# Kernel optimization log

Measured on AMD Instinct MI355X. Metric: run time of the kernel, lower is better.

The kernel has to match this reference:

```python
import jax, jax.numpy as jnp
import numpy as np

B, L, E = 16, 2048, 256


def setup_inputs() -> dict:
    key = jax.random.key(0)
    ks = jax.random.split(key, 8)
    s = 1.0 / np.sqrt(E)
    x = jax.random.normal(ks[0], (B, L, E), dtype=jnp.float32)
    lengths = jax.random.randint(ks[1], (B,), 0, L, dtype=jnp.int32)
    Wq = jax.random.normal(ks[2], (E, E), dtype=jnp.float32) * s
    bq = jax.random.normal(ks[3], (E,), dtype=jnp.float32) * s
    Wk = jax.random.normal(ks[4], (E, E), dtype=jnp.float32) * s
    bk = jax.random.normal(ks[5], (E,), dtype=jnp.float32) * s
    Wv = jax.random.normal(ks[6], (E, E), dtype=jnp.float32) * s
    bv = jax.random.normal(ks[7], (E,), dtype=jnp.float32) * s
    return {"x": x, "lengths": lengths, "Wq": Wq, "bq": bq,
            "Wk": Wk, "bk": bk, "Wv": Wv, "bv": bv}


def reference(x, lengths, Wq, bq, Wk, bk, Wv, bv):
    # ragged validity mask: [B, L, 1]
    mask = (jnp.arange(L)[None, :] < lengths[:, None]).astype(x.dtype)[..., None]
    q = (jnp.einsum('ble,fe->blf', x, Wq) + bq) * mask  # masked queries -> zero padded output rows
    k = (jnp.einsum('ble,fe->blf', x, Wk) + bk) * mask  # masked keys -> exclude padding from contraction
    v = jnp.einsum('ble,fe->blf', x, Wv) + bv           # invalid keys already zeroed via k
    attn_weights = jnp.einsum('bqe,bke->bqk', q, k)      # [B, L, L] (no softmax in original)
    attn_output = jnp.einsum('bqk,bke->bqe', attn_weights, v)  # [B, L, E]
    # to_padded_tensor(pad=0).mean(dim=1) divides by the PADDED length L
    return attn_output.sum(axis=1) / jnp.asarray(L, x.dtype)  # [B, E]
```

## Files before the change

kernel.cpp:

```cpp
#include <hip/hip_runtime.h>

#define Bb 16
#define Ll 2048
#define Ee 256
#define E4 64
#define BPB 32
#define RPB 64
#define JT 16
#define FS (Ee / JT)

#define P1_OFF 0
#define TP_OFF (P1_OFF + Bb*BPB*Ee)
#define C_OFF  (TP_OFF + Bb*JT*Ee)
#define U_OFF  (C_OFF + Bb)
#define W_OFF  (U_OFF + Bb*Ee)

__global__ void __launch_bounds__(256) k1(const float* __restrict__ x,
                                          const int* __restrict__ lengths,
                                          float* __restrict__ P1) {
    const int b = blockIdx.y, i = blockIdx.x;
    const int tid = threadIdx.x, lane = tid & 63, wid = tid >> 6;
    const int len = lengths[b];
    const int r0 = i * RPB;
    float4* slot = (float4*)(P1 + ((size_t)(b * BPB + i)) * Ee);
    if (r0 >= len) {
        if (tid < 64) slot[tid] = make_float4(0.f, 0.f, 0.f, 0.f);
        return;
    }
    const float4* xb = (const float4*)(x + (size_t)b * Ll * Ee);
    float4 acc = {0.f, 0.f, 0.f, 0.f};
#pragma unroll
    for (int rr = 0; rr < 16; ++rr) {
        const int r = r0 + wid + rr * 4;
        float4 v = xb[(size_t)r * E4 + lane];
        const bool ok = (r < len);
        acc.x += ok ? v.x : 0.f; acc.y += ok ? v.y : 0.f;
        acc.z += ok ? v.z : 0.f; acc.w += ok ? v.w : 0.f;
    }
    __shared__ float4 part[256];
    part[tid] = acc;
    __syncthreads();
    if (tid < 64) {
        float4 a = part[tid], b1 = part[64+tid], c1 = part[128+tid], d1 = part[192+tid];
        slot[tid] = make_float4(a.x+b1.x+c1.x+d1.x, a.y+b1.y+c1.y+d1.y,
                                a.z+b1.z+c1.z+d1.z, a.w+b1.w+c1.w+d1.w);
    }
}

__global__ void __launch_bounds__(256) k2(const float* __restrict__ P1,
                                          const int* __restrict__ lengths,
                                          const float* __restrict__ Wq,
                                          const float* __restrict__ bq,
                                          const float* __restrict__ Wk,
                                          const float* __restrict__ bk,
                                          float* __restrict__ TP, float* __restrict__ C,
                                          float* __restrict__ U, float* __restrict__ W) {
    const int b = blockIdx.y, j = blockIdx.x;
    const int tid = threadIdx.x;
    const int len = lengths[b];
    __shared__ alignas(16) float xs[Ee];
    __shared__ alignas(16) float s_sh[Ee];
    {
        const float* P = P1 + (size_t)b * BPB * Ee + tid;
        float a0 = 0.f, a1 = 0.f, a2 = 0.f, a3 = 0.f;
#pragma unroll
        for (int q = 0; q < BPB; q += 4) {
            a0 += P[(size_t)(q+0) * Ee];
            a1 += P[(size_t)(q+1) * Ee];
            a2 += P[(size_t)(q+2) * Ee];
            a3 += P[(size_t)(q+3) * Ee];
        }
        xs[tid] = (a0 + a1) + (a2 + a3);
    }
    __syncthreads();
    {
        const float4* wrow = (const float4*)(Wq + (size_t)tid * Ee);
        const float4* x4   = (const float4*)xs;
        float acc = 0.f;
#pragma unroll 8
        for (int q = 0; q < E4; ++q) {
            float4 w = wrow[q]; float4 v = x4[q];
            acc += w.x*v.x + w.y*v.y + w.z*v.z + w.w*v.w;
        }
        s_sh[tid] = acc + (float)len * bq[tid];
    }
    __syncthreads();
    float tp = 0.f;
#pragma unroll
    for (int f0 = 0; f0 < FS; ++f0) {
        const int f = j * FS + f0;
        tp += s_sh[f] * Wk[(size_t)f * Ee + tid];
    }
    TP[((size_t)(b * JT + j)) * Ee + tid] = tp;
    if (j == 0) {
        U[b * Ee + tid] = 0.f;
        float p = s_sh[tid] * bk[tid];
#pragma unroll
        for (int m = 32; m; m >>= 1) p += __shfl_xor(p, m, 64);
        __shared__ float cred[4];
        if ((tid & 63) == 0) cred[tid >> 6] = p;
        __syncthreads();
        if (tid == 0) { C[b] = cred[0] + cred[1] + cred[2] + cred[3]; W[b] = 0.f; }
    }
}

__global__ void __launch_bounds__(256) k3(const float* __restrict__ x,
                                          const int* __restrict__ lengths,
                                          const float* __restrict__ TP,
                                          const float* __restrict__ C,
                                          float* __restrict__ U, float* __restrict__ W) {
    const int b = blockIdx.y, i = blockIdx.x;
    const int len = lengths[b];
    const int r0 = i * RPB;
    if (r0 >= len) return;
    const int tid = threadIdx.x, lane = tid & 63, wid = tid >> 6;
    const float4* tp4 = (const float4*)(TP + (size_t)b * JT * Ee);
    float4 tv = {0.f, 0.f, 0.f, 0.f};
#pragma unroll
    for (int jj = 0; jj < JT; ++jj) {
        float4 t = tp4[jj * E4 + lane];
        tv.x += t.x; tv.y += t.y; tv.z += t.z; tv.w += t.w;
    }
    const float cb = C[b];
    const float4* xb = (const float4*)(x + (size_t)b * Ll * Ee);
    float4 uacc = {0.f, 0.f, 0.f, 0.f};
    float wacc = 0.f;
#pragma unroll
    for (int rr = 0; rr < 16; ++rr) {
        const int r = r0 + wid + rr * 4;
        float4 xv = xb[(size_t)r * E4 + lane];
        float d = xv.x*tv.x + xv.y*tv.y + xv.z*tv.z + xv.w*tv.w;
#pragma unroll
        for (int m = 32; m; m >>= 1) d += __shfl_xor(d, m, 64);
        float w = (r < len) ? (d + cb) : 0.f;
        uacc.x += w*xv.x; uacc.y += w*xv.y; uacc.z += w*xv.z; uacc.w += w*xv.w;
        wacc += w;
    }
    __shared__ float4 part[256];
    __shared__ float cw[4];
    part[tid] = uacc;
    if (lane == 0) cw[wid] = wacc;
    __syncthreads();
    if (tid < 64) {
        float4 a = part[tid], b1 = part[64+tid], c1 = part[128+tid], d1 = part[192+tid];
        float* ub = U + b * Ee + tid * 4;
        atomicAdd(ub + 0, a.x + b1.x + c1.x + d1.x);
        atomicAdd(ub + 1, a.y + b1.y + c1.y + d1.y);
        atomicAdd(ub + 2, a.z + b1.z + c1.z + d1.z);
        atomicAdd(ub + 3, a.w + b1.w + c1.w + d1.w);
    }
    if (tid == 0) atomicAdd(W + b, cw[0] + cw[1] + cw[2] + cw[3]);
}

__global__ void __launch_bounds__(256) k4(const float* __restrict__ U,
                                          const float* __restrict__ W,
                                          const float* __restrict__ Wv,
                                          const float* __restrict__ bv,
                                          float* __restrict__ out) {
    const int b = blockIdx.y, j = blockIdx.x;
    const int tid = threadIdx.x, lane = tid & 63, wid = tid >> 6;
    __shared__ float4 u4[E4];
    __shared__ float red[4][64];
    if (tid < E4) u4[tid] = ((const float4*)(U + b * Ee))[tid];
    __syncthreads();
    const int e = j * 64 + lane;
    const float4* wv = (const float4*)(Wv + (size_t)e * Ee);
    float acc = 0.f;
#pragma unroll
    for (int q = 0; q < 16; ++q) {
        float4 w = wv[wid * 16 + q]; float4 v = u4[wid * 16 + q];
        acc += w.x*v.x + w.y*v.y + w.z*v.z + w.w*v.w;
    }
    red[wid][lane] = acc;
    __syncthreads();
    if (wid == 0) {
        float r = red[0][lane] + red[1][lane] + red[2][lane] + red[3][lane];
        out[b * Ee + e] = (r + bv[e] * W[b]) * (1.0f / (float)Ll);
    }
}

extern "C" void kernel_launch(void* const* d_in, const int* in_sizes, int n_in,
                              void* d_out, int out_size, void* d_ws, size_t ws_size,
                              hipStream_t stream) {
    const float* x       = (const float*)d_in[0];
    const int*   lengths = (const int*)d_in[1];
    const float* Wq      = (const float*)d_in[2];
    const float* bq      = (const float*)d_in[3];
    const float* Wk      = (const float*)d_in[4];
    const float* bk      = (const float*)d_in[5];
    const float* Wv      = (const float*)d_in[6];
    const float* bv      = (const float*)d_in[7];
    float* out = (float*)d_out;
    float* ws  = (float*)d_ws;

    k1<<<dim3(BPB, Bb), 256, 0, stream>>>(x, lengths, ws + P1_OFF);
    k2<<<dim3(JT, Bb), 256, 0, stream>>>(ws + P1_OFF, lengths, Wq, bq, Wk, bk,
                                         ws + TP_OFF, ws + C_OFF, ws + U_OFF, ws + W_OFF);
    k3<<<dim3(BPB, Bb), 256, 0, stream>>>(x, lengths, ws + TP_OFF, ws + C_OFF,
                                          ws + U_OFF, ws + W_OFF);
    k4<<<dim3(4, Bb), 256, 0, stream>>>(ws + U_OFF, ws + W_OFF, Wv, bv, out);
}
```

Baseline: 31.66 us.

## Fuse value projection into row-reduction kernel and accumulate output atomically

Merges the per-batch U reduction kernel and the Wv projection kernel: each active row-block now reduces its partial U in shared memory, multiplies it by Wv itself, and atomically adds its scaled contribution into the output, which k1 zeroes. This removes one kernel launch and the intermediate U/W round-trip. In exchange every active block reads the full 256x256 Wv matrix (mostly from L2) and issues 256 atomics to the output. JT is doubled to spread the Wk stage over more blocks, and an unroll factor is raised.

```diff
diff --git a/kernel.cpp b/kernel.cpp
--- a/kernel.cpp
+++ b/kernel.cpp
@@ -6,20 +6,20 @@
 #define E4 64
 #define BPB 32
 #define RPB 64
-#define JT 16
+#define JT 32
 #define FS (Ee / JT)
 
 #define P1_OFF 0
 #define TP_OFF (P1_OFF + Bb*BPB*Ee)
 #define C_OFF  (TP_OFF + Bb*JT*Ee)
-#define U_OFF  (C_OFF + Bb)
-#define W_OFF  (U_OFF + Bb*Ee)
 
 __global__ void __launch_bounds__(256) k1(const float* __restrict__ x,
                                           const int* __restrict__ lengths,
-                                          float* __restrict__ P1) {
+                                          float* __restrict__ P1,
+                                          float* __restrict__ out) {
     const int b = blockIdx.y, i = blockIdx.x;
     const int tid = threadIdx.x, lane = tid & 63, wid = tid >> 6;
+    if (i == 0) out[b * Ee + tid] = 0.f;
     const int len = lengths[b];
     const int r0 = i * RPB;
     float4* slot = (float4*)(P1 + ((size_t)(b * BPB + i)) * Ee);
@@ -53,8 +53,7 @@
                                           const float* __restrict__ bq,
                                           const float* __restrict__ Wk,
                                           const float* __restrict__ bk,
-                                          float* __restrict__ TP, float* __restrict__ C,
-                                          float* __restrict__ U, float* __restrict__ W) {
+                                          float* __restrict__ TP, float* __restrict__ C) {
     const int b = blockIdx.y, j = blockIdx.x;
     const int tid = threadIdx.x;
     const int len = lengths[b];
@@ -77,7 +76,7 @@
         const float4* wrow = (const float4*)(Wq + (size_t)tid * Ee);
         const float4* x4   = (const float4*)xs;
         float acc = 0.f;
-#pragma unroll 8
+#pragma unroll 16
         for (int q = 0; q < E4; ++q) {
             float4 w = wrow[q]; float4 v = x4[q];
             acc += w.x*v.x + w.y*v.y + w.z*v.z + w.w*v.w;
@@ -93,32 +92,34 @@
     }
     TP[((size_t)(b * JT + j)) * Ee + tid] = tp;
     if (j == 0) {
-        U[b * Ee + tid] = 0.f;
         float p = s_sh[tid] * bk[tid];
 #pragma unroll
         for (int m = 32; m; m >>= 1) p += __shfl_xor(p, m, 64);
         __shared__ float cred[4];
         if ((tid & 63) == 0) cred[tid >> 6] = p;
         __syncthreads();
-        if (tid == 0) { C[b] = cred[0] + cred[1] + cred[2] + cred[3]; W[b] = 0.f; }
+        if (tid == 0) C[b] = cred[0] + cred[1] + cred[2] + cred[3];
     }
 }
 
-__global__ void __launch_bounds__(256) k3(const float* __restrict__ x,
-                                          const int* __restrict__ lengths,
-                                          const float* __restrict__ TP,
-                                          const float* __restrict__ C,
-                                          float* __restrict__ U, float* __restrict__ W) {
+__global__ void __launch_bounds__(256) k34(const float* __restrict__ x,
+                                           const int* __restrict__ lengths,
+                                           const float* __restrict__ TP,
+                                           const float* __restrict__ C,
+                                           const float* __restrict__ Wv,
+                                           const float* __restrict__ bv,
+                                           float* __restrict__ out) {
     const int b = blockIdx.y, i = blockIdx.x;
     const int len = lengths[b];
     const int r0 = i * RPB;
     if (r0 >= len) return;
     const int tid = threadIdx.x, lane = tid & 63, wid = tid >> 6;
+
     const float4* tp4 = (const float4*)(TP + (size_t)b * JT * Ee);
     float4 tv = {0.f, 0.f, 0.f, 0.f};
 #pragma unroll
     for (int jj = 0; jj < JT; ++jj) {
-        float4 t = tp4[jj * E4 + lane];
+        float4 t = tp4[(size_t)jj * E4 + lane];
         tv.x += t.x; tv.y += t.y; tv.z += t.z; tv.w += t.w;
     }
     const float cb = C[b];
@@ -138,45 +139,33 @@
     }
     __shared__ float4 part[256];
     __shared__ float cw[4];
+    __shared__ alignas(16) float u_sh[Ee];
+    __shared__ float w_sh;
     part[tid] = uacc;
     if (lane == 0) cw[wid] = wacc;
     __syncthreads();
     if (tid < 64) {
         float4 a = part[tid], b1 = part[64+tid], c1 = part[128+tid], d1 = part[192+tid];
-        float* ub = U + b * Ee + tid * 4;
-        atomicAdd(ub + 0, a.x + b1.x + c1.x + d1.x);
-        atomicAdd(ub + 1, a.y + b1.y + c1.y + d1.y);
-        atomicAdd(ub + 2, a.z + b1.z + c1.z + d1.z);
-        atomicAdd(ub + 3, a.w + b1.w + c1.w + d1.w);
+        ((float4*)u_sh)[tid] = make_float4(a.x+b1.x+c1.x+d1.x, a.y+b1.y+c1.y+d1.y,
+                                           a.z+b1.z+c1.z+d1.z, a.w+b1.w+c1.w+d1.w);
     }
-    if (tid == 0) atomicAdd(W + b, cw[0] + cw[1] + cw[2] + cw[3]);
-}
+    if (tid == 0) w_sh = cw[0] + cw[1] + cw[2] + cw[3];
+    __syncthreads();
 
-__global__ void __launch_bounds__(256) k4(const float* __restrict__ U,
-                                          const float* __restrict__ W,
-                                          const float* __restrict__ Wv,
-                                          const float* __restrict__ bv,
-                                          float* __restrict__ out) {
-    const int b = blockIdx.y, j = blockIdx.x;
-    const int tid = threadIdx.x, lane = tid & 63, wid = tid >> 6;
-    __shared__ float4 u4[E4];
-    __shared__ float red[4][64];
-    if (tid < E4) u4[tid] = ((const float4*)(U + b * Ee))[tid];
-    __syncthreads();
-    const int e = j * 64 + lane;
-    const float4* wv = (const float4*)(Wv + (size_t)e * Ee);
-    float acc = 0.f;
+    const float4* wrow = (const float4*)(Wv + (size_t)tid * Ee);
+    const float4* u4   = (const float4*)u_sh;
+    float acc0 = 0.f, acc1 = 0.f, acc2 = 0.f, acc3 = 0.f;
 #pragma unroll
-    for (int q = 0; q < 16; ++q) {
-        float4 w = wv[wid * 16 + q]; float4 v = u4[wid * 16 + q];
-        acc += w.x*v.x + w.y*v.y + w.z*v.z + w.w*v.w;
+    for (int q = 0; q < E4; q += 4) {
+        float4 w0 = wrow[q+0], w1 = wrow[q+1], w2 = wrow[q+2], w3 = wrow[q+3];
+        float4 v0 = u4[q+0],  v1 = u4[q+1],  v2 = u4[q+2],  v3 = u4[q+3];
+        acc0 += w0.x*v0.x + w0.y*v0.y + w0.z*v0.z + w0.w*v0.w;
+        acc1 += w1.x*v1.x + w1.y*v1.y + w1.z*v1.z + w1.w*v1.w;
+        acc2 += w2.x*v2.x + w2.y*v2.y + w2.z*v2.z + w2.w*v2.w;
+        acc3 += w3.x*v3.x + w3.y*v3.y + w3.z*v3.z + w3.w*v3.w;
     }
-    red[wid][lane] = acc;
-    __syncthreads();
-    if (wid == 0) {
-        float r = red[0][lane] + red[1][lane] + red[2][lane] + red[3][lane];
-        out[b * Ee + e] = (r + bv[e] * W[b]) * (1.0f / (float)Ll);
-    }
+    float acc = (acc0 + acc1) + (acc2 + acc3);
+    atomicAdd(out + b * Ee + tid, (acc + bv[tid] * w_sh) * (1.0f / (float)Ll));
 }
 
 extern "C" void kernel_launch(void* const* d_in, const int* in_sizes, int n_in,
@@ -193,10 +182,9 @@
     float* out = (float*)d_out;
     float* ws  = (float*)d_ws;
 
-    k1<<<dim3(BPB, Bb), 256, 0, stream>>>(x, lengths, ws + P1_OFF);
+    k1<<<dim3(BPB, Bb), 256, 0, stream>>>(x, lengths, ws + P1_OFF, out);
     k2<<<dim3(JT, Bb), 256, 0, stream>>>(ws + P1_OFF, lengths, Wq, bq, Wk, bk,
-                                         ws + TP_OFF, ws + C_OFF, ws + U_OFF, ws + W_OFF);
-    k3<<<dim3(BPB, Bb), 256, 0, stream>>>(x, lengths, ws + TP_OFF, ws + C_OFF,
-                                          ws + U_OFF, ws + W_OFF);
-    k4<<<dim3(4, Bb), 256, 0, stream>>>(ws + U_OFF, ws + W_OFF, Wv, bv, out);
+                                         ws + TP_OFF, ws + C_OFF);
+    k34<<<dim3(BPB, Bb), 256, 0, stream>>>(x, lengths, ws + TP_OFF, ws + C_OFF,
+                                           Wv, bv, out);
 }
```

After: 48.90 us. +54.5%, slower.

## Fuse projection kernel into row-weighting kernel, recompute per block

Applied to the files above, without the earlier changes.

Merges the small k2 (Wq and Wk projections of the masked row sum) into k3, so every active row block recomputes s and the transposed projection itself and no intermediate TP/C buffers are needed. The zeroing of U and W moves into k1. This removes one kernel launch and the global round trip through TP, but makes each block redo the 256x256 matvecs against Wq and Wk, which adds redundant compute and L2 traffic per block.

```diff
diff --git a/kernel.cpp b/kernel.cpp
--- a/kernel.cpp
+++ b/kernel.cpp
@@ -6,20 +6,22 @@
 #define E4 64
 #define BPB 32
 #define RPB 64
-#define JT 16
-#define FS (Ee / JT)
 
 #define P1_OFF 0
-#define TP_OFF (P1_OFF + Bb*BPB*Ee)
-#define C_OFF  (TP_OFF + Bb*JT*Ee)
-#define U_OFF  (C_OFF + Bb)
+#define U_OFF  (P1_OFF + Bb*BPB*Ee)
 #define W_OFF  (U_OFF + Bb*Ee)
 
 __global__ void __launch_bounds__(256) k1(const float* __restrict__ x,
                                           const int* __restrict__ lengths,
-                                          float* __restrict__ P1) {
+                                          float* __restrict__ P1,
+                                          float* __restrict__ U,
+                                          float* __restrict__ W) {
     const int b = blockIdx.y, i = blockIdx.x;
     const int tid = threadIdx.x, lane = tid & 63, wid = tid >> 6;
+    if (i == 0) {
+        U[b * Ee + tid] = 0.f;
+        if (tid == 0) W[b] = 0.f;
+    }
     const int len = lengths[b];
     const int r0 = i * RPB;
     float4* slot = (float4*)(P1 + ((size_t)(b * BPB + i)) * Ee);
@@ -47,19 +49,26 @@
     }
 }
 
-__global__ void __launch_bounds__(256) k2(const float* __restrict__ P1,
-                                          const int* __restrict__ lengths,
-                                          const float* __restrict__ Wq,
-                                          const float* __restrict__ bq,
-                                          const float* __restrict__ Wk,
-                                          const float* __restrict__ bk,
-                                          float* __restrict__ TP, float* __restrict__ C,
-                                          float* __restrict__ U, float* __restrict__ W) {
-    const int b = blockIdx.y, j = blockIdx.x;
-    const int tid = threadIdx.x;
+__global__ void __launch_bounds__(256) k23(const float* __restrict__ x,
+                                           const int* __restrict__ lengths,
+                                           const float* __restrict__ P1,
+                                           const float* __restrict__ Wq,
+                                           const float* __restrict__ bq,
+                                           const float* __restrict__ Wk,
+                                           const float* __restrict__ bk,
+                                           float* __restrict__ U,
+                                           float* __restrict__ W) {
+    const int b = blockIdx.y, i = blockIdx.x;
     const int len = lengths[b];
+    const int r0 = i * RPB;
+    if (r0 >= len) return;
+    const int tid = threadIdx.x, lane = tid & 63, wid = tid >> 6;
+
     __shared__ alignas(16) float xs[Ee];
     __shared__ alignas(16) float s_sh[Ee];
+    __shared__ float4 tred[4][64];
+    __shared__ float cred[4];
+
     {
         const float* P = P1 + (size_t)b * BPB * Ee + tid;
         float a0 = 0.f, a1 = 0.f, a2 = 0.f, a3 = 0.f;
@@ -73,11 +82,12 @@
         xs[tid] = (a0 + a1) + (a2 + a3);
     }
     __syncthreads();
+
     {
         const float4* wrow = (const float4*)(Wq + (size_t)tid * Ee);
         const float4* x4   = (const float4*)xs;
         float acc = 0.f;
-#pragma unroll 8
+#pragma unroll 16
         for (int q = 0; q < E4; ++q) {
             float4 w = wrow[q]; float4 v = x4[q];
             acc += w.x*v.x + w.y*v.y + w.z*v.z + w.w*v.w;
@@ -85,43 +95,33 @@
         s_sh[tid] = acc + (float)len * bq[tid];
     }
     __syncthreads();
-    float tp = 0.f;
-#pragma unroll
-    for (int f0 = 0; f0 < FS; ++f0) {
-        const int f = j * FS + f0;
-        tp += s_sh[f] * Wk[(size_t)f * Ee + tid];
-    }
-    TP[((size_t)(b * JT + j)) * Ee + tid] = tp;
-    if (j == 0) {
-        U[b * Ee + tid] = 0.f;
+
+    {
+        const float4* wk4 = (const float4*)Wk;
+        float4 tacc = {0.f, 0.f, 0.f, 0.f};
+#pragma unroll 16
+        for (int q = 0; q < 64; ++q) {
+            const int f = wid * 64 + q;
+            const float s = s_sh[f];
+            const float4 w4 = wk4[(size_t)f * E4 + lane];
+            tacc.x += s * w4.x; tacc.y += s * w4.y;
+            tacc.z += s * w4.z; tacc.w += s * w4.w;
+        }
+        tred[wid][lane] = tacc;
         float p = s_sh[tid] * bk[tid];
 #pragma unroll
         for (int m = 32; m; m >>= 1) p += __shfl_xor(p, m, 64);
-        __shared__ float cred[4];
-        if ((tid & 63) == 0) cred[tid >> 6] = p;
-        __syncthreads();
-        if (tid == 0) { C[b] = cred[0] + cred[1] + cred[2] + cred[3]; W[b] = 0.f; }
-    }
-}
-
-__global__ void __launch_bounds__(256) k3(const float* __restrict__ x,
-                                          const int* __restrict__ lengths,
-                                          const float* __restrict__ TP,
-                                          const float* __restrict__ C,
-                                          float* __restrict__ U, float* __restrict__ W) {
-    const int b = blockIdx.y, i = blockIdx.x;
-    const int len = lengths[b];
-    const int r0 = i * RPB;
-    if (r0 >= len) return;
-    const int tid = threadIdx.x, lane = tid & 63, wid = tid >> 6;
-    const float4* tp4 = (const float4*)(TP + (size_t)b * JT * Ee);
-    float4 tv = {0.f, 0.f, 0.f, 0.f};
-#pragma unroll
-    for (int jj = 0; jj < JT; ++jj) {
-        float4 t = tp4[jj * E4 + lane];
-        tv.x += t.x; tv.y += t.y; tv.z += t.z; tv.w += t.w;
-    }
-    const float cb = C[b];
+        if (lane == 0) cred[wid] = p;
+    }
+    __syncthreads();
+
+    float4 tv;
+    {
+        float4 a = tred[0][lane], b1 = tred[1][lane], c1 = tred[2][lane], d1 = tred[3][lane];
+        tv.x = a.x+b1.x+c1.x+d1.x; tv.y = a.y+b1.y+c1.y+d1.y;
+        tv.z = a.z+b1.z+c1.z+d1.z; tv.w = a.w+b1.w+c1.w+d1.w;
+    }
+    const float cb = cred[0] + cred[1] + cred[2] + cred[3];
     const float4* xb = (const float4*)(x + (size_t)b * Ll * Ee);
     float4 uacc = {0.f, 0.f, 0.f, 0.f};
     float wacc = 0.f;
@@ -193,10 +193,8 @@
     float* out = (float*)d_out;
     float* ws  = (float*)d_ws;
 
-    k1<<<dim3(BPB, Bb), 256, 0, stream>>>(x, lengths, ws + P1_OFF);
-    k2<<<dim3(JT, Bb), 256, 0, stream>>>(ws + P1_OFF, lengths, Wq, bq, Wk, bk,
-                                         ws + TP_OFF, ws + C_OFF, ws + U_OFF, ws + W_OFF);
-    k3<<<dim3(BPB, Bb), 256, 0, stream>>>(x, lengths, ws + TP_OFF, ws + C_OFF,
-                                          ws + U_OFF, ws + W_OFF);
+    k1<<<dim3(BPB, Bb), 256, 0, stream>>>(x, lengths, ws + P1_OFF, ws + U_OFF, ws + W_OFF);
+    k23<<<dim3(BPB, Bb), 256, 0, stream>>>(x, lengths, ws + P1_OFF, Wq, bq, Wk, bk,
+                                           ws + U_OFF, ws + W_OFF);
     k4<<<dim3(4, Bb), 256, 0, stream>>>(ws + U_OFF, ws + W_OFF, Wv, bv, out);
 }
```

Measured after the change: 38.61 us. 21.9% more time.

## Precompute Wq^T·Wk product in row-sum kernel to shorten the serial chain

Applied to the files above, without the earlier changes.

Adds 256 extra blocks to the first kernel that compute M = Wq^T·Wk, plus bq·Wk, Wq^T·bk and bq·bk. These blocks run concurrently with the per-batch row-sum reduction, which is batch-independent work. The second kernel then needs only a single matvec against M instead of two dependent matvecs with Wq and Wk, removing a barrier and a serial dependency from it. In exchange it adds a 256x256x256 weight product and an extra 256 KB matrix read per batch in the second kernel.

```diff
diff --git a/kernel.cpp b/kernel.cpp
--- a/kernel.cpp
+++ b/kernel.cpp
@@ -14,54 +14,113 @@
 #define C_OFF  (TP_OFF + Bb*JT*Ee)
 #define U_OFF  (C_OFF + Bb)
 #define W_OFF  (U_OFF + Bb*Ee)
-
-__global__ void __launch_bounds__(256) k1(const float* __restrict__ x,
-                                          const int* __restrict__ lengths,
-                                          float* __restrict__ P1) {
-    const int b = blockIdx.y, i = blockIdx.x;
-    const int tid = threadIdx.x, lane = tid & 63, wid = tid >> 6;
-    const int len = lengths[b];
-    const int r0 = i * RPB;
-    float4* slot = (float4*)(P1 + ((size_t)(b * BPB + i)) * Ee);
-    if (r0 >= len) {
-        if (tid < 64) slot[tid] = make_float4(0.f, 0.f, 0.f, 0.f);
-        return;
-    }
-    const float4* xb = (const float4*)(x + (size_t)b * Ll * Ee);
-    float4 acc = {0.f, 0.f, 0.f, 0.f};
-#pragma unroll
-    for (int rr = 0; rr < 16; ++rr) {
-        const int r = r0 + wid + rr * 4;
-        float4 v = xb[(size_t)r * E4 + lane];
-        const bool ok = (r < len);
-        acc.x += ok ? v.x : 0.f; acc.y += ok ? v.y : 0.f;
-        acc.z += ok ? v.z : 0.f; acc.w += ok ? v.w : 0.f;
-    }
-    __shared__ float4 part[256];
-    part[tid] = acc;
-    __syncthreads();
-    if (tid < 64) {
-        float4 a = part[tid], b1 = part[64+tid], c1 = part[128+tid], d1 = part[192+tid];
-        slot[tid] = make_float4(a.x+b1.x+c1.x+d1.x, a.y+b1.y+c1.y+d1.y,
-                                a.z+b1.z+c1.z+d1.z, a.w+b1.w+c1.w+d1.w);
-    }
-}
-
-__global__ void __launch_bounds__(256) k2(const float* __restrict__ P1,
+#define M_OFF  (W_OFF + Bb)
+#define BQK_OFF (M_OFF + Ee*Ee)
+#define KV_OFF  (BQK_OFF + Ee)
+#define BETA_OFF (KV_OFF + Ee)
+
+__global__ void __launch_bounds__(256) kA(const float* __restrict__ x,
                                           const int* __restrict__ lengths,
                                           const float* __restrict__ Wq,
                                           const float* __restrict__ bq,
                                           const float* __restrict__ Wk,
                                           const float* __restrict__ bk,
-                                          float* __restrict__ TP, float* __restrict__ C,
-                                          float* __restrict__ U, float* __restrict__ W) {
+                                          float* __restrict__ ws) {
+    const int blk = blockIdx.x;
+    const int tid = threadIdx.x, lane = tid & 63, wid = tid >> 6;
+
+    if (blk < Bb * BPB) {
+        const int b = blk >> 5, i = blk & 31;
+        const int len = lengths[b];
+        const int r0 = i * RPB;
+        float4* slot = (float4*)(ws + P1_OFF + ((size_t)(b * BPB + i)) * Ee);
+        if (r0 >= len) {
+            if (tid < 64) slot[tid] = make_float4(0.f, 0.f, 0.f, 0.f);
+            return;
+        }
+        const float4* xb = (const float4*)(x + (size_t)b * Ll * Ee);
+        float4 acc = {0.f, 0.f, 0.f, 0.f};
+#pragma unroll
+        for (int rr = 0; rr < 16; ++rr) {
+            const int r = r0 + wid + rr * 4;
+            float4 v = xb[(size_t)r * E4 + lane];
+            const bool ok = (r < len);
+            acc.x += ok ? v.x : 0.f; acc.y += ok ? v.y : 0.f;
+            acc.z += ok ? v.z : 0.f; acc.w += ok ? v.w : 0.f;
+        }
+        __shared__ float4 part[256];
+        part[tid] = acc;
+        __syncthreads();
+        if (tid < 64) {
+            float4 a = part[tid], b1 = part[64+tid], c1 = part[128+tid], d1 = part[192+tid];
+            slot[tid] = make_float4(a.x+b1.x+c1.x+d1.x, a.y+b1.y+c1.y+d1.y,
+                                    a.z+b1.z+c1.z+d1.z, a.w+b1.w+c1.w+d1.w);
+        }
+        return;
+    }
+
+    const int ep = blk - Bb * BPB;
+    const float4* wk4 = (const float4*)Wk;
+    float4 macc = {0.f, 0.f, 0.f, 0.f};
+    float4 qacc = {0.f, 0.f, 0.f, 0.f};
+    const bool doBqk = (ep == 0);
+#pragma unroll 16
+    for (int q = 0; q < 64; ++q) {
+        const int f = wid * 64 + q;
+        const float wq = Wq[(size_t)f * Ee + ep];
+        const float4 w4 = wk4[(size_t)f * E4 + lane];
+        macc.x += wq * w4.x; macc.y += wq * w4.y;
+        macc.z += wq * w4.z; macc.w += wq * w4.w;
+        if (doBqk) {
+            const float bqf = bq[f];
+            qacc.x += bqf * w4.x; qacc.y += bqf * w4.y;
+            qacc.z += bqf * w4.z; qacc.w += bqf * w4.w;
+        }
+    }
+    float kv = Wq[(size_t)(wid * 64 + lane) * Ee + ep] * bk[wid * 64 + lane];
+#pragma unroll
+    for (int m = 32; m; m >>= 1) kv += __shfl_xor(kv, m, 64);
+
+    __shared__ float4 mred[4][64];
+    __shared__ float4 qred[4][64];
+    __shared__ float kred[4];
+    mred[wid][lane] = macc;
+    if (doBqk) qred[wid][lane] = qacc;
+    if (lane == 0) kred[wid] = kv;
+    __syncthreads();
+    if (wid == 0) {
+        float4 a = mred[0][lane], b1 = mred[1][lane], c1 = mred[2][lane], d1 = mred[3][lane];
+        ((float4*)(ws + M_OFF + (size_t)ep * Ee))[lane] =
+            make_float4(a.x+b1.x+c1.x+d1.x, a.y+b1.y+c1.y+d1.y,
+                        a.z+b1.z+c1.z+d1.z, a.w+b1.w+c1.w+d1.w);
+        if (lane == 0) ws[KV_OFF + ep] = kred[0] + kred[1] + kred[2] + kred[3];
+    }
+    if (doBqk) {
+        if (wid == 1) {
+            float4 a = qred[0][lane], b1 = qred[1][lane], c1 = qred[2][lane], d1 = qred[3][lane];
+            ((float4*)(ws + BQK_OFF))[lane] =
+                make_float4(a.x+b1.x+c1.x+d1.x, a.y+b1.y+c1.y+d1.y,
+                            a.z+b1.z+c1.z+d1.z, a.w+b1.w+c1.w+d1.w);
+        }
+        float p = bq[tid] * bk[tid];
+#pragma unroll
+        for (int m = 32; m; m >>= 1) p += __shfl_xor(p, m, 64);
+        __shared__ float bred[4];
+        if (lane == 0) bred[wid] = p;
+        __syncthreads();
+        if (tid == 0) ws[BETA_OFF] = bred[0] + bred[1] + bred[2] + bred[3];
+    }
+}
+
+__global__ void __launch_bounds__(256) kB(const float* __restrict__ lengths_f,
+                                          const int* __restrict__ lengths,
+                                          float* __restrict__ ws) {
     const int b = blockIdx.y, j = blockIdx.x;
     const int tid = threadIdx.x;
     const int len = lengths[b];
     __shared__ alignas(16) float xs[Ee];
-    __shared__ alignas(16) float s_sh[Ee];
     {
-        const float* P = P1 + (size_t)b * BPB * Ee + tid;
+        const float* P = ws + P1_OFF + (size_t)b * BPB * Ee + tid;
         float a0 = 0.f, a1 = 0.f, a2 = 0.f, a3 = 0.f;
 #pragma unroll
         for (int q = 0; q < BPB; q += 4) {
@@ -73,34 +132,29 @@
         xs[tid] = (a0 + a1) + (a2 + a3);
     }
     __syncthreads();
-    {
-        const float4* wrow = (const float4*)(Wq + (size_t)tid * Ee);
-        const float4* x4   = (const float4*)xs;
-        float acc = 0.f;
-#pragma unroll 8
-        for (int q = 0; q < E4; ++q) {
-            float4 w = wrow[q]; float4 v = x4[q];
-            acc += w.x*v.x + w.y*v.y + w.z*v.z + w.w*v.w;
-        }
-        s_sh[tid] = acc + (float)len * bq[tid];
-    }
-    __syncthreads();
+    const float* M = ws + M_OFF;
     float tp = 0.f;
 #pragma unroll
-    for (int f0 = 0; f0 < FS; ++f0) {
-        const int f = j * FS + f0;
-        tp += s_sh[f] * Wk[(size_t)f * Ee + tid];
-    }
-    TP[((size_t)(b * JT + j)) * Ee + tid] = tp;
+    for (int q = 0; q < FS; ++q) {
+        const int ep = j * FS + q;
+        tp += xs[ep] * M[(size_t)ep * Ee + tid];
+    }
+    if (j == 0) tp += (float)len * ws[BQK_OFF + tid];
+    ws[TP_OFF + ((size_t)(b * JT + j)) * Ee + tid] = tp;
+
     if (j == 0) {
-        U[b * Ee + tid] = 0.f;
-        float p = s_sh[tid] * bk[tid];
+        ws[U_OFF + b * Ee + tid] = 0.f;
+        float p = xs[tid] * ws[KV_OFF + tid];
 #pragma unroll
         for (int m = 32; m; m >>= 1) p += __shfl_xor(p, m, 64);
         __shared__ float cred[4];
         if ((tid & 63) == 0) cred[tid >> 6] = p;
         __syncthreads();
-        if (tid == 0) { C[b] = cred[0] + cred[1] + cred[2] + cred[3]; W[b] = 0.f; }
+        if (tid == 0) {
+            ws[C_OFF + b] = cred[0] + cred[1] + cred[2] + cred[3]
+                          + (float)len * ws[BETA_OFF];
+            ws[W_OFF + b] = 0.f;
+        }
     }
 }
 
@@ -118,7 +172,7 @@
     float4 tv = {0.f, 0.f, 0.f, 0.f};
 #pragma unroll
     for (int jj = 0; jj < JT; ++jj) {
-        float4 t = tp4[jj * E4 + lane];
+        float4 t = tp4[(size_t)jj * E4 + lane];
         tv.x += t.x; tv.y += t.y; tv.z += t.z; tv.w += t.w;
     }
     const float cb = C[b];
@@ -193,9 +247,8 @@
     float* out = (float*)d_out;
     float* ws  = (float*)d_ws;
 
-    k1<<<dim3(BPB, Bb), 256, 0, stream>>>(x, lengths, ws + P1_OFF);
-    k2<<<dim3(JT, Bb), 256, 0, stream>>>(ws + P1_OFF, lengths, Wq, bq, Wk, bk,
-                                         ws + TP_OFF, ws + C_OFF, ws + U_OFF, ws + W_OFF);
+    kA<<<Bb * BPB + Ee, 256, 0, stream>>>(x, lengths, Wq, bq, Wk, bk, ws);
+    kB<<<dim3(JT, Bb), 256, 0, stream>>>(nullptr, lengths, ws);
     k3<<<dim3(BPB, Bb), 256, 0, stream>>>(x, lengths, ws + TP_OFF, ws + C_OFF,
                                           ws + U_OFF, ws + W_OFF);
     k4<<<dim3(4, Bb), 256, 0, stream>>>(ws + U_OFF, ws + W_OFF, Wv, bv, out);
```

Result: slower. 32.38 us (+2.3%).
